# Optimization experiments

Hardware: AMD Instinct MI355X
Metric: run time of the kernel (lower is better)

The kernel has to match this reference:

```python
import jax, jax.numpy as jnp
import numpy as np
from jax import lax

B, T, D, H = 4, 4096, 1024, 8
DK, DV = 1024, 2048          # expand_k=1.0, expand_v=2.0
RANK, MAXL, LOOPD = 16, 8, 128  # lora_rank, max_loops, dim*loop_dim_fraction
THRESH = 0.99
EPS = 1e-6
GK_SCALE = 16.0              # GLA forget-gate temperature


def setup_inputs() -> dict:
    key = jax.random.key(0)
    ks = jax.random.split(key, 16)
    r = lambda i, shape, s=0.02: jax.random.normal(ks[i], shape, jnp.float32) * s
    return {
        "h": jax.random.normal(ks[0], (B, T, D), jnp.float32),
        "e": jax.random.normal(ks[1], (B, T, D), jnp.float32),
        "norm_w": jnp.ones((D,), jnp.float32),
        "out_norm_w": jnp.ones((D,), jnp.float32),
        "Wq": r(2, (D, DK)), "Wk": r(3, (D, DK)), "Wv": r(4, (D, DV)),
        "Wgk": r(5, (D, DK)), "Wg": r(6, (D, DV)), "Wo": r(7, (DV, D)),
        "lora_A": r(8, (MAXL, D, RANK)), "lora_B": r(9, (MAXL, RANK, D)),
        "inj_A": 0.9 * jnp.eye(D, dtype=jnp.float32) + r(10, (D, D)),
        "inj_B": r(11, (D, D)),
        "act_w": r(12, (D,)),
        "act_b": jnp.full((), -2.0, jnp.float32),  # gradual halting
        "loop_table": r(13, (MAXL, LOOPD)),
        "n_loops": 4,
    }


def rmsnorm(x, w):
    return x * lax.rsqrt(jnp.mean(x * x, axis=-1, keepdims=True) + EPS) * w


def gla(x, Wq, Wk, Wv, Wgk, Wg, Wo, num_heads):
    """Gated Linear Attention: data-dependent forget gates, linear-time recurrent scan."""
    b, t, d = x.shape
    dk, dv = Wq.shape[1], Wv.shape[1]
    dkh, dvh = dk // num_heads, dv // num_heads
    q = (x @ Wq).reshape(b, t, num_heads, dkh) * (dkh ** -0.5)
    k = (x @ Wk).reshape(b, t, num_heads, dkh)
    v = (x @ Wv).reshape(b, t, num_heads, dvh)
    # forget gate alpha in (0,1): exp(logsigmoid(gk)/16)
    alpha = jnp.exp(jax.nn.log_sigmoid(x @ Wgk) / GK_SCALE).reshape(b, t, num_heads, dkh)

    def step(S, qkva):  # S: (b, H, dkh, dvh)
        qt, kt, vt, at = qkva
        S = at[..., None] * S + kt[..., None] * vt[..., None, :]
        ot = jnp.einsum('bhk,bhkv->bhv', qt, S)
        return S, ot

    S0 = jnp.zeros((b, num_heads, dkh, dvh), x.dtype)
    xs = (jnp.swapaxes(q, 0, 1), jnp.swapaxes(k, 0, 1),
          jnp.swapaxes(v, 0, 1), jnp.swapaxes(alpha, 0, 1))
    _, o = lax.scan(step, S0, xs)                  # o: (t, b, H, dvh)
    o = jnp.swapaxes(o, 0, 1).reshape(b, t, dv)
    o = o * jax.nn.silu(x @ Wg)                    # output gate
    return o @ Wo


def reference(h, e, norm_w, out_norm_w, Wq, Wk, Wv, Wgk, Wg, Wo,
              lora_A, lora_B, inj_A, inj_B, act_w, act_b, loop_table, n_loops):
    b, t_len, d = h.shape
    halted = jnp.zeros((b, t_len), bool)
    cum = jnp.zeros((b, t_len), h.dtype)
    h_out = jnp.zeros_like(h)
    loopd = loop_table.shape[1]
    for t in range(n_loops):  # small fixed depth loop (structurally distinct LoRA/embed per t)
        # loop index embedding on first loopd channels
        h = h.at[..., :loopd].add(loop_table[t])
        h_norm = rmsnorm(h + e, norm_w)
        g = gla(h_norm, Wq, Wk, Wv, Wgk, Wg, Wo, H)   # dropout: eval mode (identity)
        g = g + (g @ lora_A[t]) @ lora_B[t]            # depth LoRA
        h = h @ inj_A.T + e @ inj_B.T + g              # LTI injection: A.h + B.e + gla
        # ACT halting accumulate
        p = jax.nn.sigmoid(h @ act_w + act_b)          # (b, t_len)
        running = ~halted
        p_eff = jnp.where(running, p, jnp.zeros_like(p))
        new_cum = cum + p_eff
        newly = running & (new_cum >= THRESH)
        w = jnp.where(newly, 1.0 - cum, p_eff)         # remainder for newly-halted
        h_out = h_out + w[..., None] * h
        cum = new_cum
        halted = halted | newly
    return rmsnorm(h_out, out_norm_w)
```

## Files before the change

### kernel.cpp

```cpp
#include <hip/hip_runtime.h>

#define BB 4
#define TT 4096
#define DD 1024
#define HH 8
#define DKK 1024
#define DVV 2048
#define MR (BB*TT)
#define DKH 128
#define DVH 256
#define NLOOPS 4
#define LCH 128
#define NCH (TT/LCH)
#define PADW 136
#define NPROJ 7168

#define WS_NEED 662310912ull

__device__ __attribute__((aligned(256))) unsigned char g_ws[WS_NEED];

typedef __bf16 bf16x8 __attribute__((ext_vector_type(8)));
typedef float  f32x4  __attribute__((ext_vector_type(4)));

template<int N> struct IC { static constexpr int v = N; };

__device__ __forceinline__ unsigned short f2bfu(float f) {
    unsigned int u = __builtin_bit_cast(unsigned int, f);
    u += 0x7fffu + ((u >> 16) & 1u);
    return (unsigned short)(u >> 16);
}
__device__ __forceinline__ float bfu2f(unsigned short s) {
    unsigned int u = ((unsigned int)s) << 16;
    return __builtin_bit_cast(float, u);
}

__device__ __forceinline__ void gld_lds16(const void* g, void* l) {
    __builtin_amdgcn_global_load_lds(
        (__attribute__((address_space(1))) void*)const_cast<void*>(g),
        (__attribute__((address_space(3))) void*)l, 16, 0, 0);
}

__global__ __launch_bounds__(256) void k_transpose_bf16(
    const float* __restrict__ in, unsigned short* __restrict__ out, int K, int N)
{
    __shared__ float tile[64][65];
    int k0 = blockIdx.y * 64, n0 = blockIdx.x * 64;
    int tx = threadIdx.x & 63, ty = threadIdx.x >> 6;
    #pragma unroll
    for (int r = 0; r < 64; r += 4)
        tile[ty + r][tx] = in[(size_t)(k0 + ty + r) * N + n0 + tx];
    __syncthreads();
    #pragma unroll
    for (int r = 0; r < 64; r += 4)
        out[(size_t)(n0 + ty + r) * K + k0 + tx] = f2bfu(tile[tx][ty + r]);
}

__global__ __launch_bounds__(256) void k_conv_e(
    const float* __restrict__ e, unsigned short* __restrict__ he)
{
    size_t gid = (size_t)blockIdx.x * 256 + threadIdx.x;
    size_t b4 = gid * 4;
    size_t row = b4 >> 10; int col = (int)(b4 & 1023);
    float4 v = *(const float4*)&e[row * 1024 + col];
    *(ushort4*)&he[row * 2048 + 1024 + col] =
        make_ushort4(f2bfu(v.x), f2bfu(v.y), f2bfu(v.z), f2bfu(v.w));
}

__global__ __launch_bounds__(256) void k_conv_injcomb(
    const float* __restrict__ injA, const float* __restrict__ injB,
    unsigned short* __restrict__ WinjT, float* __restrict__ diag)
{
    int idx = blockIdx.x * 256 + threadIdx.x;
    int i = idx >> 10, j = idx & 1023;
    float va = injA[idx], vb = injB[idx];
    unsigned short ua;
    if (i == j) { diag[i] = va; ua = 0; }
    else        { ua = f2bfu(va); }
    WinjT[(size_t)i * 2048 + j] = ua;
    WinjT[(size_t)i * 2048 + 1024 + j] = f2bfu(vb);
}

__global__ __launch_bounds__(256) void k_prep(
    float* __restrict__ h, const float* __restrict__ e,
    const float* __restrict__ norm_w, const float* __restrict__ ltab,
    unsigned short* __restrict__ he, unsigned short* __restrict__ xn_bf)
{
    int row = blockIdx.x, tid = threadIdx.x;
    size_t base = (size_t)row * DD + tid * 4;
    float4 hv = *(float4*)&h[base];
    if (tid < 32) {
        float4 lv = *(const float4*)&ltab[tid * 4];
        hv.x += lv.x; hv.y += lv.y; hv.z += lv.z; hv.w += lv.w;
        *(float4*)&h[base] = hv;
    }
    float4 ev = *(const float4*)&e[base];
    float sx = hv.x + ev.x, sy = hv.y + ev.y, sz = hv.z + ev.z, sw = hv.w + ev.w;
    float partial = sx*sx + sy*sy + sz*sz + sw*sw;
    __shared__ float red[256];
    red[tid] = partial; __syncthreads();
    for (int st = 128; st > 0; st >>= 1) {
        if (tid < st) red[tid] += red[tid + st];
        __syncthreads();
    }
    float rms = rsqrtf(red[0] * (1.0f / DD) + 1e-6f);
    float4 wv = *(const float4*)&norm_w[tid * 4];
    *(ushort4*)&xn_bf[base] = make_ushort4(
        f2bfu(sx * rms * wv.x), f2bfu(sy * rms * wv.y),
        f2bfu(sz * rms * wv.z), f2bfu(sw * rms * wv.w));
    *(ushort4*)&he[(size_t)row * 2048 + tid * 4] =
        make_ushort4(f2bfu(hv.x), f2bfu(hv.y), f2bfu(hv.z), f2bfu(hv.w));
}

#define LD_AV(CB, MH) \
    _Pragma("unroll") \
    for (int i2 = 0; i2 < 4; ++i2) { \
        const char* rp = sm + (CB) + ((MH) * 16384) \
                       + ((wm * 64 + i2 * 16 + ln15) * 128); \
        av[i2][0] = *(const bf16x8*)(rp + xc0); \
        av[i2][1] = *(const bf16x8*)(rp + xc1); \
    }
#define LD_BV(CB, NH) \
    _Pragma("unroll") \
    for (int j2 = 0; j2 < 2; ++j2) { \
        const char* rp = sm + (CB) + 32768 + ((NH) * 16384) \
                       + ((wn * 32 + j2 * 16 + ln15) * 128); \
        bv[NH][j2][0] = *(const bf16x8*)(rp + xc0); \
        bv[NH][j2][1] = *(const bf16x8*)(rp + xc1); \
    }
#define MFMA_Q(MH, NH) \
    __builtin_amdgcn_s_setprio(1); \
    _Pragma("unroll") \
    for (int i2 = 0; i2 < 4; ++i2) \
        _Pragma("unroll") \
        for (int j2 = 0; j2 < 2; ++j2) { \
            acc[(MH)*4+i2][(NH)*2+j2] = __builtin_amdgcn_mfma_f32_16x16x32_bf16( \
                av[i2][0], bv[NH][j2][0], acc[(MH)*4+i2][(NH)*2+j2], 0, 0, 0); \
            acc[(MH)*4+i2][(NH)*2+j2] = __builtin_amdgcn_mfma_f32_16x16x32_bf16( \
                av[i2][1], bv[NH][j2][1], acc[(MH)*4+i2][(NH)*2+j2], 0, 0, 0); \
        } \
    __builtin_amdgcn_s_setprio(0);

template<int KB, class EPI>
__device__ __forceinline__ void gemm8_core(
    const char* __restrict__ Ab, const char* __restrict__ Bb,
    int bm, int bn, char* sm, f32x4 (&acc)[8][4], EPI&& epi)
{
    constexpr int NKT = KB / 128;
    const int tid = threadIdx.x;
    const int lane = tid & 63;
    const int wave = tid >> 6;
    const int wm = wave >> 2, wn = wave & 3;
    const int ln15 = lane & 15, q4 = lane >> 4;
    (void)q4;
    const int xorv = (ln15 & 7) << 4;
    const int xc0 = (q4 * 16) ^ xorv;
    const int xc1 = (64 + q4 * 16) ^ xorv;

    const int L0 = tid * 16;
    const int L1 = 8192 + tid * 16;
    const int lin0 = L0 ^ (((L0 >> 7) & 7) << 4);
    const int lin1 = L1 ^ (((L1 >> 7) & 7) << 4);
    const int sr0 = lin0 >> 7, sc0 = lin0 & 127;
    const int sr1 = lin1 >> 7, sc1 = lin1 & 127;

    bf16x8 av[4][2];
    bf16x8 bv[2][2][2];

    auto STAGE = [&](const char* gb, int row0, int kcol, int region) {
        gld_lds16(gb + (size_t)(row0 + sr0) * KB + (kcol + sc0), sm + region + L0);
        gld_lds16(gb + (size_t)(row0 + sr1) * KB + (kcol + sc1), sm + region + L1);
    };

    STAGE(Ab, bm,       0, 0);
    STAGE(Bb, bn,       0, 32768);
    STAGE(Bb, bn + 128, 0, 49152);
    STAGE(Ab, bm + 128, 0, 16384);

    #pragma unroll 2
    for (int kt = 0; kt < NKT - 1; ++kt) {
        const int cb = (kt & 1) << 16;
        const int sb = cb ^ 65536;
        const int kcol = (kt + 1) * 128;
        STAGE(Ab, bm, kcol, sb);
        asm volatile("s_waitcnt vmcnt(4)" ::: "memory");
        __builtin_amdgcn_s_barrier();
        LD_AV(cb, 0)
        LD_BV(cb, 0)
        LD_BV(cb, 1)
        MFMA_Q(0, 0)
        STAGE(Bb, bn, kcol, sb + 32768);
        MFMA_Q(0, 1)
        STAGE(Bb, bn + 128, kcol, sb + 49152);
        asm volatile("s_waitcnt vmcnt(6)" ::: "memory");
        __builtin_amdgcn_s_barrier();
        LD_AV(cb, 1)
        MFMA_Q(1, 1)
        STAGE(Ab, bm + 128, kcol, sb + 16384);
        MFMA_Q(1, 0)
    }
    {
        const int cb = ((NKT - 1) & 1) << 16;
        asm volatile("s_waitcnt vmcnt(2)" ::: "memory");
        __builtin_amdgcn_s_barrier();
        LD_AV(cb, 0)
        LD_BV(cb, 0)
        LD_BV(cb, 1)
        MFMA_Q(0, 0)
        epi(IC<0>{}, IC<0>{});
        MFMA_Q(0, 1)
        epi(IC<0>{}, IC<1>{});
        asm volatile("s_waitcnt vmcnt(0)" ::: "memory");
        __builtin_amdgcn_s_barrier();
        LD_AV(cb, 1)
        MFMA_Q(1, 1)
        epi(IC<1>{}, IC<1>{});
        MFMA_Q(1, 0)
        epi(IC<1>{}, IC<0>{});
    }
}

__global__ __launch_bounds__(512, 2) void k_gemm_proj8(
    const unsigned short* __restrict__ A, const unsigned short* __restrict__ Bt,
    unsigned short* __restrict__ qout, unsigned short* __restrict__ kout,
    float* __restrict__ lgout, unsigned short* __restrict__ vout,
    unsigned short* __restrict__ xgout, float qscale)
{
    extern __shared__ char sm[];
    int bid = blockIdx.x;
    int nb = (bid & 7) * 224 + (bid >> 3);
    int bm = (nb / 28) * 256, bn = (nb % 28) * 256;

    const int tid = threadIdx.x, lane = tid & 63, wave = tid >> 6;
    const int wm = wave >> 2, wn = wave & 3;
    const int ln15 = lane & 15, q4 = lane >> 4;

    const bool islg = (bn >= 2048 && bn < 3072);
    const int lgc = bn - 2048;
    unsigned short* obuf = qout; int stride = 1024, cbc = bn;
    float scale = 1.f;
    if (bn < 1024)          { scale = qscale; }
    else if (bn < 2048)     { obuf = kout;  cbc = bn - 1024; }
    else if (bn >= 5120)    { obuf = xgout; stride = 2048; cbc = bn - 5120; }
    else if (bn >= 3072)    { obuf = vout;  stride = 2048; cbc = bn - 3072; }

    f32x4 acc[8][4];
    #pragma unroll
    for (int i = 0; i < 8; ++i)
        #pragma unroll
        for (int j = 0; j < 4; ++j) { f32x4 z = {0,0,0,0}; acc[i][j] = z; }

    auto epi = [&](auto MHt, auto NHt) {
        constexpr int mh = decltype(MHt)::v;
        constexpr int nh = decltype(NHt)::v;
        if (islg) {
            #pragma unroll
            for (int i2 = 0; i2 < 4; ++i2) {
                int rowb = bm + mh * 128 + wm * 64 + i2 * 16 + q4 * 4;
                #pragma unroll
                for (int j2 = 0; j2 < 2; ++j2) {
                    int col = lgc + nh * 128 + wn * 32 + j2 * 16 + ln15;
                    #pragma unroll
                    for (int r = 0; r < 4; ++r) {
                        float v = acc[mh * 4 + i2][nh * 2 + j2][r];
                        v = (fminf(v, 0.f) - log1pf(expf(-fabsf(v)))) * 0.0625f;
                        lgout[(size_t)(rowb + r) * 1024 + col] = v;
                    }
                }
            }
        } else {
            #pragma unroll
            for (int i2 = 0; i2 < 4; ++i2) {
                int rowb = bm + mh * 128 + wm * 64 + i2 * 16 + q4 * 4;
                #pragma unroll
                for (int j2 = 0; j2 < 2; ++j2) {
                    int col = cbc + nh * 128 + wn * 32 + j2 * 16 + ln15;
                    #pragma unroll
                    for (int r = 0; r < 4; ++r)
                        obuf[(size_t)(rowb + r) * stride + col] =
                            f2bfu(acc[mh * 4 + i2][nh * 2 + j2][r] * scale);
                }
            }
        }
    };

    gemm8_core<2048>((const char*)A, (const char*)Bt, bm, bn, sm, acc, epi);
}

template<int HASADD, int HASDIAG, int KB>
__global__ __launch_bounds__(512, 2) void k_gemm8_f32(
    const unsigned short* __restrict__ A, const unsigned short* __restrict__ Bt,
    float* __restrict__ out, const float* __restrict__ addend,
    const float* __restrict__ hsrc, const float* __restrict__ diag, int N)
{
    extern __shared__ char sm[];
    int bid = blockIdx.x;
    int cpx = gridDim.x >> 3;
    int nb = (bid & 7) * cpx + (bid >> 3);
    int nbn = N >> 8;
    int bm = (nb / nbn) * 256, bn = (nb % nbn) * 256;

    const int tid = threadIdx.x, lane = tid & 63, wave = tid >> 6;
    const int wm = wave >> 2, wn = wave & 3;
    const int ln15 = lane & 15, q4 = lane >> 4;

    f32x4 acc[8][4];
    #pragma unroll
    for (int i = 0; i < 8; ++i)
        #pragma unroll
        for (int j = 0; j < 4; ++j) { f32x4 z = {0,0,0,0}; acc[i][j] = z; }

    auto epi = [&](auto MHt, auto NHt) {
        constexpr int mh = decltype(MHt)::v;
        constexpr int nh = decltype(NHt)::v;
        #pragma unroll
        for (int i2 = 0; i2 < 4; ++i2) {
            int rowb = bm + mh * 128 + wm * 64 + i2 * 16 + q4 * 4;
            #pragma unroll
            for (int j2 = 0; j2 < 2; ++j2) {
                int col = bn + nh * 128 + wn * 32 + j2 * 16 + ln15;
                float dg = 0.f;
                if (HASDIAG) dg = diag[col];
                #pragma unroll
                for (int r = 0; r < 4; ++r) {
                    size_t oi = (size_t)(rowb + r) * N + col;
                    float v = acc[mh * 4 + i2][nh * 2 + j2][r];
                    if (HASDIAG) v += hsrc[oi] * dg;
                    if (HASADD)  v += addend[oi];
                    out[oi] = v;
                }
            }
        }
    };

    gemm8_core<KB>((const char*)A, (const char*)Bt, bm, bn, sm, acc, epi);
}

#undef LD_AV
#undef LD_BV
#undef MFMA_Q

__global__ __launch_bounds__(256) void k_c1(
    const float* __restrict__ lg, unsigned short* __restrict__ q,
    unsigned short* __restrict__ kk, float* __restrict__ dLe)
{
    int chunk = blockIdx.x;
    int bh = blockIdx.y * 2 + (threadIdx.x >> 7);
    int b = bh >> 3, h = bh & 7;
    int i = threadIdx.x & 127;
    size_t r0 = (size_t)b * TT + (size_t)chunk * LCH;
    float c = 0.f, e = 1.f;
    for (int t = 0; t < LCH; ++t) {
        size_t off = (r0 + t) * DKK + h * DKH + i;
        c += lg[off];
        e = __expf(c);
        float ei = __expf(-c);
        q[off] = f2bfu(bfu2f(q[off]) * e);
        kk[off] = f2bfu(bfu2f(kk[off]) * ei);
    }
    dLe[((size_t)chunk * 32 + bh) * DKH + i] = e;
}

__global__ __launch_bounds__(512, 1) void k_c2(
    const unsigned short* __restrict__ q, const unsigned short* __restrict__ kk,
    const unsigned short* __restrict__ v, unsigned short* __restrict__ ob,
    float* __restrict__ U)
{
    extern __shared__ unsigned short smd[];
    unsigned short* lQ  = smd;
    unsigned short* lK  = smd + LCH * PADW;
    unsigned short* lKT = smd + 2 * LCH * PADW;
    unsigned short* lVT = smd + 3 * LCH * PADW;

    int chunk = blockIdx.x, bh = blockIdx.y;
    int b = bh >> 3, h = bh & 7;
    int tid = threadIdx.x, lane = tid & 63, wave = tid >> 6;
    int wm = wave >> 2, wn = wave & 3;
    int quad = lane >> 4, mr = lane & 15;
    size_t r0 = (size_t)b * TT + (size_t)chunk * LCH;

    #pragma unroll
    for (int ps = 0; ps < 4; ++ps) {
        int idx = ps * 512 + tid;
        int row = idx >> 4, c8 = (idx & 15) * 8;
        size_t g = (r0 + row) * DKK + h * DKH + c8;
        *(int4*)&lQ[row * PADW + c8] = *(const int4*)&q[g];
        union { int4 w; unsigned short u[8]; } tmp;
        tmp.w = *(const int4*)&kk[g];
        *(int4*)&lK[row * PADW + c8] = tmp.w;
        #pragma unroll
        for (int u2 = 0; u2 < 8; ++u2)
            lKT[(c8 + u2) * PADW + row] = tmp.u[u2];
    }
    __syncthreads();

    f32x4 pa[4][2];
    #pragma unroll
    for (int i = 0; i < 4; ++i)
        #pragma unroll
        for (int j = 0; j < 2; ++j) { f32x4 z = {0,0,0,0}; pa[i][j] = z; }
    for (int k0 = 0; k0 < DKH; k0 += 32) {
        bf16x8 av[4], bvv[2];
        #pragma unroll
        for (int t2 = 0; t2 < 4; ++t2)
            av[t2] = *(const bf16x8*)&lQ[(wm * 64 + t2 * 16 + mr) * PADW + k0 + quad * 8];
        #pragma unroll
        for (int tn = 0; tn < 2; ++tn)
            bvv[tn] = *(const bf16x8*)&lK[(wn * 32 + tn * 16 + mr) * PADW + k0 + quad * 8];
        #pragma unroll
        for (int tm = 0; tm < 4; ++tm)
            #pragma unroll
            for (int tn = 0; tn < 2; ++tn)
                pa[tm][tn] = __builtin_amdgcn_mfma_f32_16x16x32_bf16(
                    av[tm], bvv[tn], pa[tm][tn], 0, 0, 0);
    }
    __syncthreads();

    #pragma unroll
    for (int tm = 0; tm < 4; ++tm)
        #pragma unroll
        for (int tn = 0; tn < 2; ++tn)
            #pragma unroll
            for (int r = 0; r < 4; ++r) {
                int trow = wm * 64 + tm * 16 + quad * 4 + r;
                int scol = wn * 32 + tn * 16 + mr;
                float pv = (trow >= scol) ? pa[tm][tn][r] : 0.f;
                lQ[trow * PADW + scol] = f2bfu(pv);
            }
    #pragma unroll
    for (int ps = 0; ps < 4; ++ps) {
        int idx = ps * 512 + tid;
        int s = idx >> 4, j8 = (idx & 15) * 8;
        size_t g = (r0 + s) * DVV + h * DVH + j8;
        union { int4 w; unsigned short u[8]; } tmp;
        tmp.w = *(const int4*)&v[g];
        #pragma unroll
        for (int u2 = 0; u2 < 8; ++u2)
            lVT[(j8 + u2) * PADW + s] = tmp.u[u2];
    }
    __syncthreads();

    #pragma unroll 1
    for (int panel = 0; panel < 2; ++panel) {
        f32x4 oa[4][2], ua[4][2];
        #pragma unroll
        for (int i = 0; i < 4; ++i)
            #pragma unroll
            for (int j = 0; j < 2; ++j) { f32x4 z = {0,0,0,0}; oa[i][j] = z; ua[i][j] = z; }
        for (int k0 = 0; k0 < LCH; k0 += 32) {
            bf16x8 pv[4], kt[4], vb[2];
            #pragma unroll
            for (int t2 = 0; t2 < 4; ++t2) {
                pv[t2] = *(const bf16x8*)&lQ [(wm * 64 + t2 * 16 + mr) * PADW + k0 + quad * 8];
                kt[t2] = *(const bf16x8*)&lKT[(wm * 64 + t2 * 16 + mr) * PADW + k0 + quad * 8];
            }
            #pragma unroll
            for (int tn = 0; tn < 2; ++tn)
                vb[tn] = *(const bf16x8*)&lVT[(wn * 32 + tn * 16 + mr) * PADW + k0 + quad * 8];
            #pragma unroll
            for (int tm = 0; tm < 4; ++tm)
                #pragma unroll
                for (int tn = 0; tn < 2; ++tn) {
                    oa[tm][tn] = __builtin_amdgcn_mfma_f32_16x16x32_bf16(
                        pv[tm], vb[tn], oa[tm][tn], 0, 0, 0);
                    ua[tm][tn] = __builtin_amdgcn_mfma_f32_16x16x32_bf16(
                        kt[tm], vb[tn], ua[tm][tn], 0, 0, 0);
                }
        }
        #pragma unroll
        for (int tm = 0; tm < 4; ++tm)
            #pragma unroll
            for (int tn = 0; tn < 2; ++tn)
                #pragma unroll
                for (int r = 0; r < 4; ++r) {
                    int m_ = wm * 64 + tm * 16 + quad * 4 + r;
                    int j_ = panel * 128 + wn * 32 + tn * 16 + mr;
                    ob[(r0 + m_) * DVV + h * DVH + j_] = f2bfu(oa[tm][tn][r]);
                    U[(((size_t)chunk * 32 + bh) * DKH + m_) * DVH + j_] = ua[tm][tn][r];
                }
        __syncthreads();
        if (panel == 0) {
            #pragma unroll
            for (int ps = 0; ps < 4; ++ps) {
                int idx = ps * 512 + tid;
                int s = idx >> 4, j8 = (idx & 15) * 8;
                size_t g = (r0 + s) * DVV + h * DVH + 128 + j8;
                union { int4 w; unsigned short u[8]; } tmp;
                tmp.w = *(const int4*)&v[g];
                #pragma unroll
                for (int u2 = 0; u2 < 8; ++u2)
                    lVT[(j8 + u2) * PADW + s] = tmp.u[u2];
            }
            __syncthreads();
        }
    }
}

__global__ __launch_bounds__(256) void k_c3(
    float* __restrict__ U, const float* __restrict__ dLe)
{
    int gid = blockIdx.x * 256 + threadIdx.x;
    int bh = gid >> 13;
    int rem = gid & 8191;
    int i = rem >> 6, j4 = rem & 63;
    float4 S = make_float4(0.f, 0.f, 0.f, 0.f);
    for (int c = 0; c < NCH; ++c) {
        size_t off = (((size_t)c * 32 + bh) * DKH + i) * DVH + j4 * 4;
        float4 u = *(float4*)&U[off];
        *(float4*)&U[off] = S;
        float d = dLe[((size_t)c * 32 + bh) * DKH + i];
        S.x = d * (S.x + u.x); S.y = d * (S.y + u.y);
        S.z = d * (S.z + u.z); S.w = d * (S.w + u.w);
    }
}

__global__ __launch_bounds__(256, 1) void k_c4(
    const unsigned short* __restrict__ q, const float* __restrict__ S,
    unsigned short* __restrict__ ob, const unsigned short* __restrict__ xg)
{
    extern __shared__ unsigned short smd[];
    unsigned short* lQ  = smd;
    unsigned short* lST = smd + LCH * PADW;

    int chunk = blockIdx.x, bh = blockIdx.y;
    int b = bh >> 3, h = bh & 7;
    int tid = threadIdx.x, lane = tid & 63, wave = tid >> 6;
    int wm = wave >> 1, wn = wave & 1;
    int quad = lane >> 4, mr = lane & 15;
    size_t r0 = (size_t)b * TT + (size_t)chunk * LCH;

    #pragma unroll
    for (int ps = 0; ps < 8; ++ps) {
        int idx = ps * 256 + tid;
        int row = idx >> 4, c8 = (idx & 15) * 8;
        size_t g = (r0 + row) * DKK + h * DKH + c8;
        *(int4*)&lQ[row * PADW + c8] = *(const int4*)&q[g];
    }

    #pragma unroll 1
    for (int panel = 0; panel < 2; ++panel) {
        __syncthreads();
        #pragma unroll
        for (int ps = 0; ps < 16; ++ps) {
            int idx = ps * 256 + tid;
            int i = idx >> 5, j4 = idx & 31;
            float4 sv = *(const float4*)&S[(((size_t)chunk * 32 + bh) * DKH + i) * DVH
                                           + panel * 128 + j4 * 4];
            lST[(j4 * 4 + 0) * PADW + i] = f2bfu(sv.x);
            lST[(j4 * 4 + 1) * PADW + i] = f2bfu(sv.y);
            lST[(j4 * 4 + 2) * PADW + i] = f2bfu(sv.z);
            lST[(j4 * 4 + 3) * PADW + i] = f2bfu(sv.w);
        }
        __syncthreads();

        f32x4 oa[4][4];
        #pragma unroll
        for (int i = 0; i < 4; ++i)
            #pragma unroll
            for (int j = 0; j < 4; ++j) { f32x4 z = {0,0,0,0}; oa[i][j] = z; }
        for (int k0 = 0; k0 < DKH; k0 += 32) {
            bf16x8 av[4], bvv[4];
            #pragma unroll
            for (int t2 = 0; t2 < 4; ++t2) {
                av[t2] = *(const bf16x8*)&lQ [(wm * 64 + t2 * 16 + mr) * PADW + k0 + quad * 8];
                bvv[t2] = *(const bf16x8*)&lST[(wn * 64 + t2 * 16 + mr) * PADW + k0 + quad * 8];
            }
            #pragma unroll
            for (int tm = 0; tm < 4; ++tm)
                #pragma unroll
                for (int tn = 0; tn < 4; ++tn)
                    oa[tm][tn] = __builtin_amdgcn_mfma_f32_16x16x32_bf16(
                        av[tm], bvv[tn], oa[tm][tn], 0, 0, 0);
        }
        #pragma unroll
        for (int tm = 0; tm < 4; ++tm)
            #pragma unroll
            for (int tn = 0; tn < 4; ++tn)
                #pragma unroll
                for (int r = 0; r < 4; ++r) {
                    int t_ = wm * 64 + tm * 16 + quad * 4 + r;
                    int j_ = panel * 128 + wn * 64 + tn * 16 + mr;
                    size_t oi = (r0 + t_) * DVV + h * DVH + j_;
                    float ov = bfu2f(ob[oi]) + oa[tm][tn][r];
                    float xf = bfu2f(xg[oi]);
                    ob[oi] = f2bfu(ov * xf / (1.f + expf(-xf)));
                }
    }
}

__global__ __launch_bounds__(256) void k_lora1(
    const float* __restrict__ G, const float* __restrict__ A, float* __restrict__ tmp)
{
    int row = blockIdx.x * 4 + (threadIdx.x >> 6);
    int lane = threadIdx.x & 63;
    float acc[16];
    #pragma unroll
    for (int r = 0; r < 16; ++r) acc[r] = 0.f;
    const float* grow = G + (size_t)row * DD;
    for (int k2 = lane; k2 < DD; k2 += 64) {
        float g = grow[k2];
        const float4* ar = (const float4*)(A + k2 * 16);
        float4 a0 = ar[0], a1 = ar[1], a2 = ar[2], a3 = ar[3];
        acc[0] = fmaf(g, a0.x, acc[0]);  acc[1] = fmaf(g, a0.y, acc[1]);
        acc[2] = fmaf(g, a0.z, acc[2]);  acc[3] = fmaf(g, a0.w, acc[3]);
        acc[4] = fmaf(g, a1.x, acc[4]);  acc[5] = fmaf(g, a1.y, acc[5]);
        acc[6] = fmaf(g, a1.z, acc[6]);  acc[7] = fmaf(g, a1.w, acc[7]);
        acc[8] = fmaf(g, a2.x, acc[8]);  acc[9] = fmaf(g, a2.y, acc[9]);
        acc[10] = fmaf(g, a2.z, acc[10]); acc[11] = fmaf(g, a2.w, acc[11]);
        acc[12] = fmaf(g, a3.x, acc[12]); acc[13] = fmaf(g, a3.y, acc[13]);
        acc[14] = fmaf(g, a3.z, acc[14]); acc[15] = fmaf(g, a3.w, acc[15]);
    }
    #pragma unroll
    for (int off = 32; off >= 1; off >>= 1)
        #pragma unroll
        for (int r = 0; r < 16; ++r) acc[r] += __shfl_xor(acc[r], off);
    if (lane == 0) {
        #pragma unroll
        for (int r = 0; r < 16; ++r) tmp[(size_t)row * 16 + r] = acc[r];
    }
}

__global__ __launch_bounds__(256) void k_lora2(
    float* __restrict__ G, const float* __restrict__ tmp, const float* __restrict__ Bm)
{
    int row = blockIdx.x, tid = threadIdx.x;
    __shared__ float t16[16];
    if (tid < 16) t16[tid] = tmp[(size_t)row * 16 + tid];
    __syncthreads();
    size_t base = (size_t)row * DD + tid * 4;
    float4 acc = *(float4*)&G[base];
    #pragma unroll
    for (int r = 0; r < 16; ++r) {
        float tv = t16[r];
        float4 bv = *(const float4*)&Bm[r * DD + tid * 4];
        acc.x = fmaf(tv, bv.x, acc.x); acc.y = fmaf(tv, bv.y, acc.y);
        acc.z = fmaf(tv, bv.z, acc.z); acc.w = fmaf(tv, bv.w, acc.w);
    }
    *(float4*)&G[base] = acc;
}

__global__ __launch_bounds__(256) void k_act(
    const float* __restrict__ h, const float* __restrict__ act_w,
    const float* __restrict__ act_b, float* __restrict__ out,
    float* __restrict__ cum, int* __restrict__ halted)
{
    int row = blockIdx.x, tid = threadIdx.x;
    size_t base = (size_t)row * DD + tid * 4;
    float4 hv = *(const float4*)&h[base];
    float4 wv = *(const float4*)&act_w[tid * 4];
    float partial = hv.x*wv.x + hv.y*wv.y + hv.z*wv.z + hv.w*wv.w;
    __shared__ float red[256];
    __shared__ float s_cm;
    __shared__ int s_hl;
    if (tid == 0) { s_cm = cum[row]; s_hl = halted[row]; }
    red[tid] = partial; __syncthreads();
    for (int st = 128; st > 0; st >>= 1) {
        if (tid < st) red[tid] += red[tid + st];
        __syncthreads();
    }
    float p = 1.f / (1.f + expf(-(red[0] + act_b[0])));
    float cm = s_cm;
    int hl = s_hl;
    float p_eff = hl ? 0.f : p;
    float ncum = cm + p_eff;
    int newly = (!hl) && (ncum >= 0.99f);
    float w = newly ? (1.f - cm) : p_eff;
    float4 ho = *(float4*)&out[base];
    ho.x += w * hv.x; ho.y += w * hv.y; ho.z += w * hv.z; ho.w += w * hv.w;
    *(float4*)&out[base] = ho;
    if (tid == 0) { cum[row] = ncum; halted[row] = hl | newly; }
}

__global__ __launch_bounds__(256) void k_final(
    float* __restrict__ io, const float* __restrict__ w)
{
    int row = blockIdx.x, tid = threadIdx.x;
    size_t base = (size_t)row * DD + tid * 4;
    float4 hv = *(const float4*)&io[base];
    float partial = hv.x*hv.x + hv.y*hv.y + hv.z*hv.z + hv.w*hv.w;
    __shared__ float red[256];
    red[tid] = partial; __syncthreads();
    for (int st = 128; st > 0; st >>= 1) {
        if (tid < st) red[tid] += red[tid + st];
        __syncthreads();
    }
    float rms = rsqrtf(red[0] * (1.0f / DD) + 1e-6f);
    float4 wv = *(const float4*)&w[tid * 4];
    float4 o = make_float4(hv.x*rms*wv.x, hv.y*rms*wv.y, hv.z*rms*wv.z, hv.w*rms*wv.w);
    *(float4*)&io[base] = o;
}

extern "C" void kernel_launch(void* const* d_in, const int* in_sizes, int n_in,
                              void* d_out, int out_size, void* d_ws, size_t ws_size,
                              hipStream_t stream)
{
    const float* in_h       = (const float*)d_in[0];
    const float* in_e       = (const float*)d_in[1];
    const float* norm_w     = (const float*)d_in[2];
    const float* out_norm_w = (const float*)d_in[3];
    const float* Wq   = (const float*)d_in[4];
    const float* Wk   = (const float*)d_in[5];
    const float* Wv   = (const float*)d_in[6];
    const float* Wgk  = (const float*)d_in[7];
    const float* Wg   = (const float*)d_in[8];
    const float* Wo   = (const float*)d_in[9];
    const float* lora_A = (const float*)d_in[10];
    const float* lora_B = (const float*)d_in[11];
    const float* inj_A  = (const float*)d_in[12];
    const float* inj_B  = (const float*)d_in[13];
    const float* act_w  = (const float*)d_in[14];
    const float* act_b  = (const float*)d_in[15];
    const float* loop_table = (const float*)d_in[16];

    char* p;
    if (ws_size >= WS_NEED) {
        p = (char*)d_ws;
    } else {
        void* sym = nullptr;
        hipGetSymbolAddress(&sym, HIP_SYMBOL(g_ws));
        p = (char*)sym;
    }

    float* h      = (float*)p;            p += (size_t)MR * DD * 4;
    unsigned short* he_bf = (unsigned short*)p; p += (size_t)MR * 2048 * 2;
    unsigned short* xn_bf = (unsigned short*)p; p += (size_t)MR * DD * 2;
    unsigned short* q_bf  = (unsigned short*)p; p += (size_t)MR * DKK * 2;
    unsigned short* k_bf  = (unsigned short*)p; p += (size_t)MR * DKK * 2;
    unsigned short* v_bf  = (unsigned short*)p; p += (size_t)MR * DVV * 2;
    unsigned short* xg_bf = (unsigned short*)p; p += (size_t)MR * DVV * 2;
    float* lgbuf  = (float*)p;            p += (size_t)MR * DKK * 4;
    unsigned short* ob0   = (unsigned short*)p; p += (size_t)MR * DVV * 2;
    float* U      = (float*)p;            p += (size_t)NCH * 32 * DKH * DVH * 4;
    float* dLe    = (float*)p;            p += (size_t)NCH * 32 * DKH * 4;
    unsigned short* WprojT = (unsigned short*)p; p += (size_t)NPROJ * DKK * 2;
    unsigned short* WoT    = (unsigned short*)p; p += (size_t)DD * DVV * 2;
    unsigned short* WinjT  = (unsigned short*)p; p += (size_t)DD * 2048 * 2;
    float* diagA = (float*)p;             p += DD * 4;
    float* tmp16 = (float*)p;             p += (size_t)MR * 16 * 4;
    float* cum   = (float*)p;             p += MR * 4;
    int*   halted = (int*)p;              p += MR * 4;
    float* g2 = lgbuf;
    float* h_out = (float*)d_out;

    hipMemcpyAsync(h, in_h, (size_t)MR * DD * 4, hipMemcpyDeviceToDevice, stream);
    hipMemsetAsync(h_out, 0, (size_t)MR * DD * 4, stream);
    hipMemsetAsync(cum, 0, MR * 4, stream);
    hipMemsetAsync(halted, 0, MR * 4, stream);

    k_transpose_bf16<<<dim3(16, 16), 256, 0, stream>>>(Wq,  WprojT,              DD, DKK);
    k_transpose_bf16<<<dim3(16, 16), 256, 0, stream>>>(Wk,  WprojT + 1024*1024,  DD, DKK);
    k_transpose_bf16<<<dim3(16, 16), 256, 0, stream>>>(Wgk, WprojT + 2048*1024,  DD, DKK);
    k_transpose_bf16<<<dim3(32, 16), 256, 0, stream>>>(Wv,  WprojT + 3072*1024,  DD, DVV);
    k_transpose_bf16<<<dim3(32, 16), 256, 0, stream>>>(Wg,  WprojT + (size_t)5120*1024, DD, DVV);
    k_transpose_bf16<<<dim3(16, 32), 256, 0, stream>>>(Wo,  WoT, DVV, DD);
    k_conv_injcomb<<<4096, 256, 0, stream>>>(inj_A, inj_B, WinjT, diagA);
    k_conv_e<<<MR * DD / 1024, 256, 0, stream>>>(in_e, he_bf);

    const float qscale = 0.08838834764831845f;

    for (int t = 0; t < NLOOPS; ++t) {
        k_prep<<<MR, 256, 0, stream>>>(h, in_e, norm_w, loop_table + t * 128, he_bf, xn_bf);

        k_gemm_proj8<<<1792, 512, 131072, stream>>>(
            xn_bf, WprojT, q_bf, k_bf, lgbuf, v_bf, xg_bf, qscale);

        k_c1<<<dim3(NCH, 16), 256, 0, stream>>>(lgbuf, q_bf, k_bf, dLe);
        k_c2<<<dim3(NCH, 32), 512, 4 * LCH * PADW * 2, stream>>>(
            q_bf, k_bf, v_bf, ob0, U);
        k_c3<<<1024, 256, 0, stream>>>(U, dLe);
        k_c4<<<dim3(NCH, 32), 256, 2 * LCH * PADW * 2, stream>>>(q_bf, U, ob0, xg_bf);

        k_gemm8_f32<0, 0, 4096><<<256, 512, 131072, stream>>>(
            ob0, WoT, g2, nullptr, nullptr, nullptr, DD);

        k_lora1<<<MR / 4, 256, 0, stream>>>(g2, lora_A + (size_t)t * DD * 16, tmp16);
        k_lora2<<<MR, 256, 0, stream>>>(g2, tmp16, lora_B + (size_t)t * 16 * DD);

        k_gemm8_f32<1, 1, 4096><<<256, 512, 131072, stream>>>(
            he_bf, WinjT, h, g2, h, diagA, DD);

        k_act<<<MR, 256, 0, stream>>>(h, act_w, act_b, h_out, cum, halted);
    }

    k_final<<<MR, 256, 0, stream>>>(h_out, out_norm_w);
}
```

Measured before the change: 4.377 ms.

## Store chunk states as bf16 in scan, move GEMM epilogues after mainloop

The inter-chunk scan kernel now writes prefix states as bf16 into a separate buffer (reusing the log-gate buffer) instead of overwriting U in fp32. The output kernel then reads these bf16 states with 16-byte loads, halving that traffic and dropping its per-element conversion. The GEMM epilogues are moved out of the pipelined mainloop so they run after all MFMAs, and the projection GEMM's stores become nontemporal. The risks are that the epilogue no longer overlaps the final MFMAs, and that the aliasing of lgbuf (also used for g2) must stay safe across kernels.

```diff
diff --git a/kernel.cpp b/kernel.cpp
--- a/kernel.cpp
+++ b/kernel.cpp
@@ -22,8 +22,6 @@
 typedef __bf16 bf16x8 __attribute__((ext_vector_type(8)));
 typedef float  f32x4  __attribute__((ext_vector_type(4)));
 
-template<int N> struct IC { static constexpr int v = N; };
-
 __device__ __forceinline__ unsigned short f2bfu(float f) {
     unsigned int u = __builtin_bit_cast(unsigned int, f);
     u += 0x7fffu + ((u >> 16) & 1u);
@@ -38,6 +36,13 @@
     __builtin_amdgcn_global_load_lds(
         (__attribute__((address_space(1))) void*)const_cast<void*>(g),
         (__attribute__((address_space(3))) void*)l, 16, 0, 0);
+}
+
+__device__ __forceinline__ void nts_u16(unsigned short* p, unsigned short v) {
+    __builtin_nontemporal_store(v, p);
+}
+__device__ __forceinline__ void nts_f32(float* p, float v) {
+    __builtin_nontemporal_store(v, p);
 }
 
 __global__ __launch_bounds__(256) void k_transpose_bf16(
@@ -140,10 +145,10 @@
         } \
     __builtin_amdgcn_s_setprio(0);
 
-template<int KB, class EPI>
+template<int KB>
 __device__ __forceinline__ void gemm8_core(
     const char* __restrict__ Ab, const char* __restrict__ Bb,
-    int bm, int bn, char* sm, f32x4 (&acc)[8][4], EPI&& epi)
+    int bm, int bn, char* sm, f32x4 (&acc)[8][4])
 {
     constexpr int NKT = KB / 128;
     const int tid = threadIdx.x;
@@ -151,7 +156,6 @@
     const int wave = tid >> 6;
     const int wm = wave >> 2, wn = wave & 3;
     const int ln15 = lane & 15, q4 = lane >> 4;
-    (void)q4;
     const int xorv = (ln15 & 7) << 4;
     const int xc0 = (q4 * 16) ^ xorv;
     const int xc1 = (64 + q4 * 16) ^ xorv;
@@ -206,16 +210,12 @@
         LD_BV(cb, 0)
         LD_BV(cb, 1)
         MFMA_Q(0, 0)
-        epi(IC<0>{}, IC<0>{});
         MFMA_Q(0, 1)
-        epi(IC<0>{}, IC<1>{});
         asm volatile("s_waitcnt vmcnt(0)" ::: "memory");
         __builtin_amdgcn_s_barrier();
         LD_AV(cb, 1)
         MFMA_Q(1, 1)
-        epi(IC<1>{}, IC<1>{});
         MFMA_Q(1, 0)
-        epi(IC<1>{}, IC<0>{});
     }
 }
 
@@ -230,60 +230,58 @@
     int nb = (bid & 7) * 224 + (bid >> 3);
     int bm = (nb / 28) * 256, bn = (nb % 28) * 256;
 
+    f32x4 acc[8][4];
+    #pragma unroll
+    for (int i = 0; i < 8; ++i)
+        #pragma unroll
+        for (int j = 0; j < 4; ++j) { f32x4 z = {0,0,0,0}; acc[i][j] = z; }
+
+    gemm8_core<2048>((const char*)A, (const char*)Bt, bm, bn, sm, acc);
+
     const int tid = threadIdx.x, lane = tid & 63, wave = tid >> 6;
     const int wm = wave >> 2, wn = wave & 3;
     const int ln15 = lane & 15, q4 = lane >> 4;
 
-    const bool islg = (bn >= 2048 && bn < 3072);
-    const int lgc = bn - 2048;
-    unsigned short* obuf = qout; int stride = 1024, cbc = bn;
-    float scale = 1.f;
-    if (bn < 1024)          { scale = qscale; }
-    else if (bn < 2048)     { obuf = kout;  cbc = bn - 1024; }
-    else if (bn >= 5120)    { obuf = xgout; stride = 2048; cbc = bn - 5120; }
-    else if (bn >= 3072)    { obuf = vout;  stride = 2048; cbc = bn - 3072; }
-
-    f32x4 acc[8][4];
-    #pragma unroll
-    for (int i = 0; i < 8; ++i)
-        #pragma unroll
-        for (int j = 0; j < 4; ++j) { f32x4 z = {0,0,0,0}; acc[i][j] = z; }
-
-    auto epi = [&](auto MHt, auto NHt) {
-        constexpr int mh = decltype(MHt)::v;
-        constexpr int nh = decltype(NHt)::v;
-        if (islg) {
-            #pragma unroll
-            for (int i2 = 0; i2 < 4; ++i2) {
-                int rowb = bm + mh * 128 + wm * 64 + i2 * 16 + q4 * 4;
+    if (bn >= 2048 && bn < 3072) {
+        int cb = bn - 2048;
+        #pragma unroll
+        for (int fm = 0; fm < 8; ++fm) {
+            int mh = fm >> 2, i2 = fm & 3;
+            int rowb = bm + mh * 128 + wm * 64 + i2 * 16 + q4 * 4;
+            #pragma unroll
+            for (int fn = 0; fn < 4; ++fn) {
+                int nh = fn >> 1, j2 = fn & 1;
+                int col = cb + nh * 128 + wn * 32 + j2 * 16 + ln15;
                 #pragma unroll
-                for (int j2 = 0; j2 < 2; ++j2) {
-                    int col = lgc + nh * 128 + wn * 32 + j2 * 16 + ln15;
-                    #pragma unroll
-                    for (int r = 0; r < 4; ++r) {
-                        float v = acc[mh * 4 + i2][nh * 2 + j2][r];
-                        v = (fminf(v, 0.f) - log1pf(expf(-fabsf(v)))) * 0.0625f;
-                        lgout[(size_t)(rowb + r) * 1024 + col] = v;
-                    }
-                }
-            }
-        } else {
-            #pragma unroll
-            for (int i2 = 0; i2 < 4; ++i2) {
-                int rowb = bm + mh * 128 + wm * 64 + i2 * 16 + q4 * 4;
-                #pragma unroll
-                for (int j2 = 0; j2 < 2; ++j2) {
-                    int col = cbc + nh * 128 + wn * 32 + j2 * 16 + ln15;
-                    #pragma unroll
-                    for (int r = 0; r < 4; ++r)
-                        obuf[(size_t)(rowb + r) * stride + col] =
-                            f2bfu(acc[mh * 4 + i2][nh * 2 + j2][r] * scale);
+                for (int r = 0; r < 4; ++r) {
+                    float v = acc[fm][fn][r];
+                    v = (fminf(v, 0.f) - log1pf(expf(-fabsf(v)))) * 0.0625f;
+                    nts_f32(&lgout[(size_t)(rowb + r) * 1024 + col], v);
                 }
             }
         }
-    };
-
-    gemm8_core<2048>((const char*)A, (const char*)Bt, bm, bn, sm, acc, epi);
+    } else {
+        unsigned short* obuf; int stride, cbc;
+        float scale = 1.f;
+        if (bn < 1024)      { obuf = qout;  stride = 1024; cbc = bn;        scale = qscale; }
+        else if (bn < 2048) { obuf = kout;  stride = 1024; cbc = bn - 1024; }
+        else if (bn < 5120) { obuf = vout;  stride = 2048; cbc = bn - 3072; }
+        else                { obuf = xgout; stride = 2048; cbc = bn - 5120; }
+        #pragma unroll
+        for (int fm = 0; fm < 8; ++fm) {
+            int mh = fm >> 2, i2 = fm & 3;
+            int rowb = bm + mh * 128 + wm * 64 + i2 * 16 + q4 * 4;
+            #pragma unroll
+            for (int fn = 0; fn < 4; ++fn) {
+                int nh = fn >> 1, j2 = fn & 1;
+                int col = cbc + nh * 128 + wn * 32 + j2 * 16 + ln15;
+                #pragma unroll
+                for (int r = 0; r < 4; ++r)
+                    nts_u16(&obuf[(size_t)(rowb + r) * stride + col],
+                            f2bfu(acc[fm][fn][r] * scale));
+            }
+        }
+    }
 }
 
 template<int HASADD, int HASDIAG, int KB>
@@ -299,40 +297,38 @@
     int nbn = N >> 8;
     int bm = (nb / nbn) * 256, bn = (nb % nbn) * 256;
 
+    f32x4 acc[8][4];
+    #pragma unroll
+    for (int i = 0; i < 8; ++i)
+        #pragma unroll
+        for (int j = 0; j < 4; ++j) { f32x4 z = {0,0,0,0}; acc[i][j] = z; }
+
+    gemm8_core<KB>((const char*)A, (const char*)Bt, bm, bn, sm, acc);
+
     const int tid = threadIdx.x, lane = tid & 63, wave = tid >> 6;
     const int wm = wave >> 2, wn = wave & 3;
     const int ln15 = lane & 15, q4 = lane >> 4;
 
-    f32x4 acc[8][4];
-    #pragma unroll
-    for (int i = 0; i < 8; ++i)
-        #pragma unroll
-        for (int j = 0; j < 4; ++j) { f32x4 z = {0,0,0,0}; acc[i][j] = z; }
-
-    auto epi = [&](auto MHt, auto NHt) {
-        constexpr int mh = decltype(MHt)::v;
-        constexpr int nh = decltype(NHt)::v;
-        #pragma unroll
-        for (int i2 = 0; i2 < 4; ++i2) {
-            int rowb = bm + mh * 128 + wm * 64 + i2 * 16 + q4 * 4;
-            #pragma unroll
-            for (int j2 = 0; j2 < 2; ++j2) {
-                int col = bn + nh * 128 + wn * 32 + j2 * 16 + ln15;
-                float dg = 0.f;
-                if (HASDIAG) dg = diag[col];
-                #pragma unroll
-                for (int r = 0; r < 4; ++r) {
-                    size_t oi = (size_t)(rowb + r) * N + col;
-                    float v = acc[mh * 4 + i2][nh * 2 + j2][r];
-                    if (HASDIAG) v += hsrc[oi] * dg;
-                    if (HASADD)  v += addend[oi];
-                    out[oi] = v;
-                }
+    #pragma unroll
+    for (int fm = 0; fm < 8; ++fm) {
+        int mh = fm >> 2, i2 = fm & 3;
+        int rowb = bm + mh * 128 + wm * 64 + i2 * 16 + q4 * 4;
+        #pragma unroll
+        for (int fn = 0; fn < 4; ++fn) {
+            int nh = fn >> 1, j2 = fn & 1;
+            int col = bn + nh * 128 + wn * 32 + j2 * 16 + ln15;
+            float dg = 0.f;
+            if (HASDIAG) dg = diag[col];
+            #pragma unroll
+            for (int r = 0; r < 4; ++r) {
+                size_t oi = (size_t)(rowb + r) * N + col;
+                float v = acc[fm][fn][r];
+                if (HASDIAG) v += hsrc[oi] * dg;
+                if (HASADD)  v += addend[oi];
+                out[oi] = v;
             }
         }
-    };
-
-    gemm8_core<KB>((const char*)A, (const char*)Bt, bm, bn, sm, acc, epi);
+    }
 }
 
 #undef LD_AV
@@ -496,7 +492,8 @@
 }
 
 __global__ __launch_bounds__(256) void k_c3(
-    float* __restrict__ U, const float* __restrict__ dLe)
+    const float* __restrict__ U, const float* __restrict__ dLe,
+    unsigned short* __restrict__ Sbf)
 {
     int gid = blockIdx.x * 256 + threadIdx.x;
     int bh = gid >> 13;
@@ -505,8 +502,9 @@
     float4 S = make_float4(0.f, 0.f, 0.f, 0.f);
     for (int c = 0; c < NCH; ++c) {
         size_t off = (((size_t)c * 32 + bh) * DKH + i) * DVH + j4 * 4;
-        float4 u = *(float4*)&U[off];
-        *(float4*)&U[off] = S;
+        float4 u = *(const float4*)&U[off];
+        *(ushort4*)&Sbf[off] = make_ushort4(
+            f2bfu(S.x), f2bfu(S.y), f2bfu(S.z), f2bfu(S.w));
         float d = dLe[((size_t)c * 32 + bh) * DKH + i];
         S.x = d * (S.x + u.x); S.y = d * (S.y + u.y);
         S.z = d * (S.z + u.z); S.w = d * (S.w + u.w);
@@ -514,7 +512,7 @@
 }
 
 __global__ __launch_bounds__(256, 1) void k_c4(
-    const unsigned short* __restrict__ q, const float* __restrict__ S,
+    const unsigned short* __restrict__ q, const unsigned short* __restrict__ Sbf,
     unsigned short* __restrict__ ob, const unsigned short* __restrict__ xg)
 {
     extern __shared__ unsigned short smd[];
@@ -527,6 +525,7 @@
     int wm = wave >> 1, wn = wave & 1;
     int quad = lane >> 4, mr = lane & 15;
     size_t r0 = (size_t)b * TT + (size_t)chunk * LCH;
+    size_t sbase = ((size_t)chunk * 32 + bh) * DKH * DVH;
 
     #pragma unroll
     for (int ps = 0; ps < 8; ++ps) {
@@ -540,15 +539,14 @@
     for (int panel = 0; panel < 2; ++panel) {
         __syncthreads();
         #pragma unroll
-        for (int ps = 0; ps < 16; ++ps) {
+        for (int ps = 0; ps < 8; ++ps) {
             int idx = ps * 256 + tid;
-            int i = idx >> 5, j4 = idx & 31;
-            float4 sv = *(const float4*)&S[(((size_t)chunk * 32 + bh) * DKH + i) * DVH
-                                           + panel * 128 + j4 * 4];
-            lST[(j4 * 4 + 0) * PADW + i] = f2bfu(sv.x);
-            lST[(j4 * 4 + 1) * PADW + i] = f2bfu(sv.y);
-            lST[(j4 * 4 + 2) * PADW + i] = f2bfu(sv.z);
-            lST[(j4 * 4 + 3) * PADW + i] = f2bfu(sv.w);
+            int i = idx >> 4, j8 = (idx & 15) * 8;
+            union { int4 w; unsigned short u[8]; } t8;
+            t8.w = *(const int4*)&Sbf[sbase + (size_t)i * DVH + panel * 128 + j8];
+            #pragma unroll
+            for (int u2 = 0; u2 < 8; ++u2)
+                lST[(j8 + u2) * PADW + i] = t8.u[u2];
         }
         __syncthreads();
 
@@ -739,6 +737,7 @@
     float* cum   = (float*)p;             p += MR * 4;
     int*   halted = (int*)p;              p += MR * 4;
     float* g2 = lgbuf;
+    unsigned short* Sbf = (unsigned short*)lgbuf;
     float* h_out = (float*)d_out;
 
     hipMemcpyAsync(h, in_h, (size_t)MR * DD * 4, hipMemcpyDeviceToDevice, stream);
@@ -766,8 +765,8 @@
         k_c1<<<dim3(NCH, 16), 256, 0, stream>>>(lgbuf, q_bf, k_bf, dLe);
         k_c2<<<dim3(NCH, 32), 512, 4 * LCH * PADW * 2, stream>>>(
             q_bf, k_bf, v_bf, ob0, U);
-        k_c3<<<1024, 256, 0, stream>>>(U, dLe);
-        k_c4<<<dim3(NCH, 32), 256, 2 * LCH * PADW * 2, stream>>>(q_bf, U, ob0, xg_bf);
+        k_c3<<<1024, 256, 0, stream>>>(U, dLe, Sbf);
+        k_c4<<<dim3(NCH, 32), 256, 2 * LCH * PADW * 2, stream>>>(q_bf, Sbf, ob0, xg_bf);
 
         k_gemm8_f32<0, 0, 4096><<<256, 512, 131072, stream>>>(
             ob0, WoT, g2, nullptr, nullptr, nullptr, DD);
```

After: 4.925 ms. 1.13x slower.
